# Performance work log

Measured on AMD Instinct MI355X. Metric: run time of the kernel, lower is better.

## Reference

```python
import jax, jax.numpy as jnp
import numpy as np

EPS = 1e-5  # torch GroupNorm default


def setup_inputs() -> dict:
    key = jax.random.key(0)
    ks = jax.random.split(key, 7)
    B, H, W, C = 8, 64, 64, 64
    x = jax.random.normal(ks[0], (B, H, W, C), dtype=jnp.float32)
    temb = jax.random.normal(ks[1], (B, 256), dtype=jnp.float32)
    scale = 0.02
    Wq = jax.random.normal(ks[2], (C, C), dtype=jnp.float32) * scale
    Wk = jax.random.normal(ks[3], (C, C), dtype=jnp.float32) * scale
    Wv = jax.random.normal(ks[4], (C, C), dtype=jnp.float32) * scale
    Wo = jax.random.normal(ks[5], (C, C), dtype=jnp.float32) * scale
    z = jnp.zeros((C,), dtype=jnp.float32)
    return {"x": x, "temb": temb, "Wq": Wq, "bq": z, "Wk": Wk, "bk": z,
            "Wv": Wv, "bv": z, "Wo": Wo, "bo": z}


def reference(x, temb, Wq, bq, Wk, bk, Wv, bv, Wo, bo):
    # x: [B, H, W, C] channels-last. temb is accepted but unused (as in source).
    B, H, W, C = x.shape
    S = H * W
    # normalize(): freshly-built GroupNorm(num_groups=1) with identity affine
    # -> standardize over all non-batch dims.
    mu = jnp.mean(x, axis=(1, 2, 3), keepdims=True)
    var = jnp.var(x, axis=(1, 2, 3), keepdims=True)
    h = (x - mu) * jax.lax.rsqrt(var + EPS)
    hf = h.reshape(B, S, C)
    q = hf @ Wq.T + bq  # [B, S, C]
    k = hf @ Wk.T + bk
    v = hf @ Wv.T + bv
    # full (S x S) score matrix, scaled by C^-0.5, naive softmax
    w = jnp.einsum('bsc,btc->bst', q, k) * (C ** -0.5)
    w = jax.nn.softmax(w, axis=-1)
    o = jnp.einsum('bst,btc->bsc', w, v)  # [B, S, C]
    o = o @ Wo.T + bo
    return x + o.reshape(B, H, W, C)
```

## Files before the change

kernel.cpp:

```cpp
#include <hip/hip_runtime.h>
#include <hip/hip_bf16.h>
#include <math.h>

#define B_ 8
#define S_ 4096
#define C_ 64
#define EPSV 1e-5f

using floatx4  = __attribute__((ext_vector_type(4)))  float;
using floatx16 = __attribute__((ext_vector_type(16))) float;
using bf16x8   = __attribute__((ext_vector_type(8)))  short;

typedef __attribute__((address_space(3))) unsigned int       as3_u32;
typedef __attribute__((address_space(1))) const unsigned int as1_u32;

__device__ __forceinline__ short f2bf(float f) {
    unsigned u = __builtin_bit_cast(unsigned, f);
    u = u + 0x7fffu + ((u >> 16) & 1u);
    return (short)(u >> 16);
}

__device__ __forceinline__ float bf2f(short s) {
    return __builtin_bit_cast(float, ((unsigned)(unsigned short)s) << 16);
}

__device__ __forceinline__ unsigned cvt_pk_bf16(float lo, float hi) {
    unsigned r;
    asm volatile("v_cvt_pk_bf16_f32 %0, %1, %2" : "=v"(r) : "v"(lo), "v"(hi));
    return r;
}

__device__ __forceinline__ void perm32swap(unsigned &a, unsigned &b) {
#if __has_builtin(__builtin_amdgcn_permlane32_swap)
    auto r = __builtin_amdgcn_permlane32_swap((int)a, (int)b, false, false);
    a = (unsigned)r[0];
    b = (unsigned)r[1];
#else
    asm volatile("v_permlane32_swap_b32 %0, %1" : "+v"(a), "+v"(b));
#endif
}

__device__ __forceinline__ bf16x8 ld_w_frag(const float* __restrict__ W, int n, int kk, int g, int c) {
    const float* p = W + (16 * n + c) * C_ + 32 * kk + 8 * g;
    bf16x8 r;
#pragma unroll
    for (int j = 0; j < 8; ++j) r[j] = f2bf(p[j]);
    return r;
}

__global__ __launch_bounds__(256) void stats1_kernel(const float* __restrict__ x,
                                                     float* __restrict__ partial) {
    int b = blockIdx.x >> 5, chunk = blockIdx.x & 31;
    const float4* xb = (const float4*)x + (size_t)b * 65536 + chunk * 2048;
    float s = 0.f, ss = 0.f;
#pragma unroll
    for (int i = 0; i < 8; ++i) {
        float4 v = xb[threadIdx.x + i * 256];
        s  += v.x + v.y + v.z + v.w;
        ss += v.x * v.x + v.y * v.y + v.z * v.z + v.w * v.w;
    }
    for (int off = 32; off > 0; off >>= 1) {
        s  += __shfl_down(s, off);
        ss += __shfl_down(ss, off);
    }
    __shared__ float sm[4], ssm[4];
    int wid = threadIdx.x >> 6, lane = threadIdx.x & 63;
    if (lane == 0) { sm[wid] = s; ssm[wid] = ss; }
    __syncthreads();
    if (threadIdx.x == 0) {
        partial[blockIdx.x * 2]     = sm[0] + sm[1] + sm[2] + sm[3];
        partial[blockIdx.x * 2 + 1] = ssm[0] + ssm[1] + ssm[2] + ssm[3];
    }
}

__global__ __launch_bounds__(512) void stats2_kernel(const float* __restrict__ partial,
                                                     float* __restrict__ stats) {
    int w = threadIdx.x >> 6, lane = threadIdx.x & 63;
    float s = 0.f, ss = 0.f;
    if (lane < 32) {
        s  = partial[(w * 32 + lane) * 2];
        ss = partial[(w * 32 + lane) * 2 + 1];
    }
    for (int off = 16; off > 0; off >>= 1) {
        s  += __shfl_down(s, off);
        ss += __shfl_down(ss, off);
    }
    if (lane == 0) {
        const float invN = 1.0f / (float)(S_ * C_);
        float mu  = s * invN;
        float var = ss * invN - mu * mu;
        stats[w * 2]     = mu;
        stats[w * 2 + 1] = rsqrtf(var + EPSV);
    }
}

__global__ __launch_bounds__(256) void proj_kernel(
    const float* __restrict__ x,
    const float* __restrict__ Wq, const float* __restrict__ bq,
    const float* __restrict__ Wk, const float* __restrict__ bk,
    const float* __restrict__ Wv, const float* __restrict__ bv,
    const float* __restrict__ stats,
    short* __restrict__ qo, char* __restrict__ kws, char* __restrict__ vws) {
    __shared__ char hbuf[8192];
    __shared__ char qimg[8192];
    __shared__ char kimg[8192];
    __shared__ char vimg[8192];

    int b  = blockIdx.x >> 6;
    int t_ = blockIdx.x & 63;
    int s0 = t_ * 64;
    float mu = stats[b * 2], rs = stats[b * 2 + 1];
    const float* xt = x + ((size_t)b * S_ + s0) * C_;
    int t = threadIdx.x;

#pragma unroll
    for (int i = 0; i < 4; ++i) {
        int fi  = t + 256 * i;
        int row = fi >> 4;
        int c4  = fi & 15;
        float4 v = *(const float4*)(xt + row * C_ + c4 * 4);
        unsigned lo = (unsigned)(unsigned short)f2bf((v.x - mu) * rs) |
                      ((unsigned)(unsigned short)f2bf((v.y - mu) * rs) << 16);
        unsigned hi = (unsigned)(unsigned short)f2bf((v.z - mu) * rs) |
                      ((unsigned)(unsigned short)f2bf((v.w - mu) * rs) << 16);
        int off = row * 128 + c4 * 8;
        off ^= (row & 7) << 4;
        *(uint2*)(hbuf + off) = make_uint2(lo, hi);
    }
    __syncthreads();

    int lane = t & 63, w = t >> 6;
    int g = lane >> 4, c = lane & 15;

    auto ld_h = [&](int row, int kcol) -> bf16x8 {
        int off = row * 128 + kcol * 2;
        off ^= (row & 7) << 4;
        return *(const bf16x8*)(hbuf + off);
    };

    bf16x8 ha[2];
    ha[0] = ld_h(16 * w + c, 8 * g);
    ha[1] = ld_h(16 * w + c, 32 + 8 * g);

    const float QSC = 0.125f * 1.44269504088896340736f;

#pragma unroll
    for (int n = 0; n < 4; ++n) {
        floatx4 aq = {0.f, 0.f, 0.f, 0.f}, ak = {0.f, 0.f, 0.f, 0.f};
#pragma unroll
        for (int kk = 0; kk < 2; ++kk) {
            bf16x8 wq = ld_w_frag(Wq, n, kk, g, c);
            bf16x8 wk = ld_w_frag(Wk, n, kk, g, c);
            aq = __builtin_amdgcn_mfma_f32_16x16x32_bf16(ha[kk], wq, aq, 0, 0, 0);
            ak = __builtin_amdgcn_mfma_f32_16x16x32_bf16(ha[kk], wk, ak, 0, 0, 0);
        }
        float bqv = bq[16 * n + c], bkv = bk[16 * n + c];
#pragma unroll
        for (int r = 0; r < 4; ++r) {
            int rr = 16 * w + 4 * g + r;
            *(short*)(qimg + rr * 128 + (16 * n + c) * 2) = f2bf((aq[r] + bqv) * QSC);
            int r32 = rr & 31;
            int koff = (r32 * 128 + (16 * n + c) * 2) ^ ((r32 & 7) << 4);
            *(short*)(kimg + (rr >> 5) * 4096 + koff) = f2bf(ak[r] + bkv);
        }
    }

    bf16x8 wv[2];
    wv[0] = ld_w_frag(Wv, w, 0, g, c);
    wv[1] = ld_w_frag(Wv, w, 1, g, c);
    float bvr[4];
#pragma unroll
    for (int r = 0; r < 4; ++r) bvr[r] = bv[16 * w + 4 * g + r];

#pragma unroll
    for (int n = 0; n < 4; ++n) {
        floatx4 av = {0.f, 0.f, 0.f, 0.f};
#pragma unroll
        for (int kk = 0; kk < 2; ++kk) {
            bf16x8 hb = ld_h(16 * n + c, 32 * kk + 8 * g);
            av = __builtin_amdgcn_mfma_f32_16x16x32_bf16(wv[kk], hb, av, 0, 0, 0);
        }
        int u   = 16 * n + c;
        int u32 = u & 31;
#pragma unroll
        for (int r = 0; r < 4; ++r) {
            int rr = 16 * w + 4 * g + r;
            int voff = (rr * 64 + u32 * 2) ^ (((rr >> 1) & 3) << 4);
            *(short*)(vimg + (u >> 5) * 4096 + voff) = f2bf(av[r] + bvr[r]);
        }
    }
    __syncthreads();

    size_t gb = ((size_t)b * 128 + 2 * t_) * 4096;
    uint4* qdst = (uint4*)(qo + ((size_t)b * S_ + s0) * C_);
#pragma unroll
    for (int i = 0; i < 2; ++i) {
        qdst[t + 256 * i] = *(const uint4*)(qimg + i * 4096 + t * 16);
        *(uint4*)(kws + gb + i * 4096 + t * 16) = *(const uint4*)(kimg + i * 4096 + t * 16);
        *(uint4*)(vws + gb + i * 4096 + t * 16) = *(const uint4*)(vimg + i * 4096 + t * 16);
    }
}

__global__ __launch_bounds__(256, 4) void flash_kernel(
    const short* __restrict__ qm, const char* __restrict__ kws, const char* __restrict__ vws,
    short* __restrict__ Opart, float2* __restrict__ mlpart) {
    __shared__ char lds[16384];

    int bid = blockIdx.x;
    int logical = (bid & 7) * 128 + (bid >> 3);
    int b = logical >> 7;
    int rest = logical & 127;
    int q0 = (rest >> 2) * 128;
    int quarter = rest & 3;
    int t = threadIdx.x;
    int lane = t & 63, w = t >> 6;
    int r5 = lane & 31, hi = lane >> 5;
    int qw = q0 + 32 * w;

    const char* kbase = kws + (size_t)b * 128 * 4096;
    const char* vbase = vws + (size_t)b * 128 * 4096;
    const short* qp = qm + (size_t)b * S_ * C_;

    bf16x8 bq[4];
#pragma unroll
    for (int kk = 0; kk < 4; ++kk)
        bq[kk] = *(const bf16x8*)(qp + (qw + r5) * C_ + 16 * kk + 8 * hi);

    floatx16 oacc[2];
#pragma unroll
    for (int mm = 0; mm < 2; ++mm)
#pragma unroll
        for (int i = 0; i < 16; ++i) oacc[mm][i] = 0.f;
    float m = -64.f, nm = 64.f, l = 0.f;

    const int kxm = (r5 & 7) << 4;
    const int vxm = ((r5 >> 1) & 3) << 4;

    auto STAGE = [&](int bi, int tt) {
        const char* gk = kbase + (size_t)tt * 4096 + t * 16;
        const char* gv = vbase + (size_t)tt * 4096 + t * 16;
        char* lk = lds +        bi * 4096 + t * 16;
        char* lv = lds + 8192 + bi * 4096 + t * 16;
        __builtin_amdgcn_global_load_lds((as1_u32*)gk, (as3_u32*)lk, 16, 0, 0);
        __builtin_amdgcn_global_load_lds((as1_u32*)gv, (as3_u32*)lv, 16, 0, 0);
    };

    auto ld_k = [&](const char* buf, int kk) -> bf16x8 {
        return *(const bf16x8*)(buf + r5 * 128 + ((32 * kk + 16 * hi) ^ kxm));
    };
    auto ld_v = [&](const char* buf, int mm, int s) -> bf16x8 {
        return *(const bf16x8*)(buf + (32 * mm + r5) * 64 + ((32 * s + 16 * hi) ^ vxm));
    };

    auto COMPUTE = [&](int bi) {
        const char* kbuf = lds +        bi * 4096;
        const char* vbuf = lds + 8192 + bi * 4096;
        floatx16 st;
#pragma unroll
        for (int i = 0; i < 16; ++i) st[i] = nm;
        __builtin_amdgcn_s_setprio(1);
#pragma unroll
        for (int kk = 0; kk < 4; ++kk) {
            bf16x8 ak = ld_k(kbuf, kk);
            st = __builtin_amdgcn_mfma_f32_32x32x16_bf16(ak, bq[kk], st, 0, 0, 0);
        }
        __builtin_amdgcn_s_setprio(0);
        bf16x8 av[2][2];
#pragma unroll
        for (int mm = 0; mm < 2; ++mm)
#pragma unroll
            for (int s = 0; s < 2; ++s)
                av[mm][s] = ld_v(vbuf, mm, s);
        float mt = st[0];
#pragma unroll
        for (int i = 1; i < 16; ++i) mt = fmaxf(mt, st[i]);
        mt = fmaxf(mt, __shfl_xor(mt, 32));
        if (!__all(mt <= 8.0f)) {
            float d = fmaxf(mt, 0.f);
            float a = __builtin_amdgcn_exp2f(-d);
            m += d;
            nm = -m;
            l *= a;
#pragma unroll
            for (int mm = 0; mm < 2; ++mm) oacc[mm] *= a;
#pragma unroll
            for (int i = 0; i < 16; ++i) st[i] -= d;
        }
        float e[16], psum = 0.f;
#pragma unroll
        for (int i = 0; i < 16; ++i) e[i] = __builtin_amdgcn_exp2f(st[i]);
#pragma unroll
        for (int i = 0; i < 16; ++i) psum += e[i];
        l += psum;
        unsigned wd[8];
#pragma unroll
        for (int j = 0; j < 8; ++j) wd[j] = cvt_pk_bf16(e[2 * j], e[2 * j + 1]);
        perm32swap(wd[0], wd[2]);
        perm32swap(wd[1], wd[3]);
        perm32swap(wd[4], wd[6]);
        perm32swap(wd[5], wd[7]);
        uint4 u0 = make_uint4(wd[0], wd[1], wd[2], wd[3]);
        uint4 u1 = make_uint4(wd[4], wd[5], wd[6], wd[7]);
        bf16x8 bp0 = __builtin_bit_cast(bf16x8, u0);
        bf16x8 bp1 = __builtin_bit_cast(bf16x8, u1);
        __builtin_amdgcn_s_setprio(1);
#pragma unroll
        for (int mm = 0; mm < 2; ++mm) {
            oacc[mm] = __builtin_amdgcn_mfma_f32_32x32x16_bf16(av[mm][0], bp0, oacc[mm], 0, 0, 0);
            oacc[mm] = __builtin_amdgcn_mfma_f32_32x32x16_bf16(av[mm][1], bp1, oacc[mm], 0, 0, 0);
        }
        __builtin_amdgcn_s_setprio(0);
    };

    const int base = quarter * 32;
    STAGE(0, base);
    __syncthreads();
    for (int r = 0; r < 32; r += 2) {
        STAGE(1, base + r + 1);
        COMPUTE(0);
        __syncthreads();
        if (r + 2 < 32) STAGE(0, base + r + 2);
        COMPUTE(1);
        __syncthreads();
    }

    l += __shfl_xor(l, 32);

    size_t prow = (size_t)(quarter * 8 + b) * S_ + q0;
    if (lane < 32)
        mlpart[prow + 32 * w + r5] = make_float2(m, l);

    short* op = Opart + (prow + 32 * w + r5) * C_;
#pragma unroll
    for (int mm = 0; mm < 2; ++mm) {
#pragma unroll
        for (int j = 0; j < 4; ++j) {
            int ch = 32 * mm + 8 * j + 4 * hi;
            uint2 u = make_uint2(cvt_pk_bf16(oacc[mm][4 * j],     oacc[mm][4 * j + 1]),
                                 cvt_pk_bf16(oacc[mm][4 * j + 2], oacc[mm][4 * j + 3]));
            *(uint2*)(op + ch) = u;
        }
    }
}

__global__ __launch_bounds__(256) void combine_kernel(
    const short* __restrict__ Opart, const float2* __restrict__ mlpart,
    const float* __restrict__ Wo, const float* __restrict__ bo,
    const float* __restrict__ x, float* __restrict__ out) {
    __shared__ char obuf[8192];

    int bid = blockIdx.x;
    int logical = (bid & 7) * 64 + (bid >> 3);
    int b = logical >> 6;
    int q0 = (logical & 63) * 64;
    int t = threadIdx.x;
    int lane = t & 63, w = t >> 6;
    int g = lane >> 4, c = lane & 15;

    const short*  P[4];
    const float2* ml[4];
#pragma unroll
    for (int h = 0; h < 4; ++h) {
        P[h]  = Opart  + ((size_t)(h * 8 + b) * S_ + q0) * C_;
        ml[h] = mlpart + (size_t)(h * 8 + b) * S_ + q0;
    }

#pragma unroll
    for (int i = 0; i < 16; ++i) {
        int idx = t + 256 * i;
        int q = idx >> 6, ch = idx & 63;
        float2 a0 = ml[0][q], a1 = ml[1][q], a2 = ml[2][q], a3 = ml[3][q];
        float M = fmaxf(fmaxf(a0.x, a1.x), fmaxf(a2.x, a3.x));
        float s0 = __builtin_amdgcn_exp2f(a0.x - M);
        float s1 = __builtin_amdgcn_exp2f(a1.x - M);
        float s2 = __builtin_amdgcn_exp2f(a2.x - M);
        float s3 = __builtin_amdgcn_exp2f(a3.x - M);
        float L  = a0.y * s0 + a1.y * s1 + a2.y * s2 + a3.y * s3;
        float o  = (bf2f(P[0][q * 64 + ch]) * s0 + bf2f(P[1][q * 64 + ch]) * s1 +
                    bf2f(P[2][q * 64 + ch]) * s2 + bf2f(P[3][q * 64 + ch]) * s3) / L;
        int off = (q * 128 + ch * 2) ^ ((q & 7) << 4);
        *(short*)(obuf + off) = f2bf(o);
    }
    __syncthreads();

    bf16x8 ao[2];
    {
        int row = 16 * w + c;
        int off0 = (row * 128 + (8 * g) * 2)      ^ ((row & 7) << 4);
        int off1 = (row * 128 + (32 + 8 * g) * 2) ^ ((row & 7) << 4);
        ao[0] = *(const bf16x8*)(obuf + off0);
        ao[1] = *(const bf16x8*)(obuf + off1);
    }
#pragma unroll
    for (int n = 0; n < 4; ++n) {
        floatx4 a = {0.f, 0.f, 0.f, 0.f};
#pragma unroll
        for (int kk = 0; kk < 2; ++kk) {
            bf16x8 bw = ld_w_frag(Wo, n, kk, g, c);
            a = __builtin_amdgcn_mfma_f32_16x16x32_bf16(ao[kk], bw, a, 0, 0, 0);
        }
        float bov = bo[16 * n + c];
#pragma unroll
        for (int r = 0; r < 4; ++r) {
            int srow = q0 + 16 * w + 4 * g + r;
            size_t idx = ((size_t)b * S_ + srow) * C_ + 16 * n + c;
            out[idx] = x[idx] + bov + a[r];
        }
    }
}

extern "C" void kernel_launch(void* const* d_in, const int* in_sizes, int n_in,
                              void* d_out, int out_size, void* d_ws, size_t ws_size,
                              hipStream_t stream) {
    const float* x  = (const float*)d_in[0];
    const float* Wq = (const float*)d_in[2];
    const float* bq = (const float*)d_in[3];
    const float* Wk = (const float*)d_in[4];
    const float* bk = (const float*)d_in[5];
    const float* Wv = (const float*)d_in[6];
    const float* bv = (const float*)d_in[7];
    const float* Wo = (const float*)d_in[8];
    const float* bo = (const float*)d_in[9];
    float* out = (float*)d_out;

    char* ws = (char*)d_ws;
    float*  partial = (float*)ws;
    float*  stats   = (float*)(ws + 2048);
    short*  q   = (short*)(ws + 4096);
    char*   kt  = (char*)(q + (size_t)B_ * S_ * C_);
    char*   vt  = kt + (size_t)B_ * 128 * 4096;
    short*  op  = (short*)(vt + (size_t)B_ * 128 * 4096);
    float2* mlp = (float2*)((char*)op + (size_t)4 * B_ * S_ * C_ * 2);

    stats1_kernel<<<256, 256, 0, stream>>>(x, partial);
    stats2_kernel<<<1, 512, 0, stream>>>(partial, stats);
    proj_kernel<<<B_ * (S_ / 64), 256, 0, stream>>>(x, Wq, bq, Wk, bk, Wv, bv, stats, q, kt, vt);
    flash_kernel<<<B_ * (S_ / 128) * 4, 256, 0, stream>>>(q, kt, vt, op, mlp);
    combine_kernel<<<B_ * (S_ / 64), 256, 0, stream>>>(op, mlp, Wo, bo, x, out);
}
```

Baseline: 80.40 us.

## Fuse split-KV combine and output projection into flash kernel via last-block counter

Removes the separate combine kernel. Each flash block now bumps an atomic counter per (batch, 128-query tile), and the last of the four KV-quarter blocks merges the partial outputs, applies Wo and bo, and adds the residual, working in two 64-row halves that reuse the flash LDS buffer. The counters are zeroed in stats1_kernel. This saves one kernel launch and lets the combine work overlap with other flash blocks, at the cost of threadfences, an atomic per block, and uneven tail work on the last-arriving blocks.

```diff
diff --git a/kernel.cpp b/kernel.cpp
--- a/kernel.cpp
+++ b/kernel.cpp
@@ -49,7 +49,9 @@
 }
 
 __global__ __launch_bounds__(256) void stats1_kernel(const float* __restrict__ x,
-                                                     float* __restrict__ partial) {
+                                                     float* __restrict__ partial,
+                                                     int* __restrict__ cnt) {
+    if (threadIdx.x == 0) cnt[blockIdx.x] = 0;
     int b = blockIdx.x >> 5, chunk = blockIdx.x & 31;
     const float4* xb = (const float4*)x + (size_t)b * 65536 + chunk * 2048;
     float s = 0.f, ss = 0.f;
@@ -203,8 +205,11 @@
 
 __global__ __launch_bounds__(256, 4) void flash_kernel(
     const short* __restrict__ qm, const char* __restrict__ kws, const char* __restrict__ vws,
-    short* __restrict__ Opart, float2* __restrict__ mlpart) {
+    short* __restrict__ Opart, float2* __restrict__ mlpart, int* __restrict__ cnt,
+    const float* __restrict__ Wo, const float* __restrict__ bo,
+    const float* __restrict__ x, float* __restrict__ out) {
     __shared__ char lds[16384];
+    __shared__ int lastflag;
 
     int bid = blockIdx.x;
     int logical = (bid & 7) * 128 + (bid >> 3);
@@ -341,21 +346,17 @@
             *(uint2*)(op + ch) = u;
         }
     }
-}
-
-__global__ __launch_bounds__(256) void combine_kernel(
-    const short* __restrict__ Opart, const float2* __restrict__ mlpart,
-    const float* __restrict__ Wo, const float* __restrict__ bo,
-    const float* __restrict__ x, float* __restrict__ out) {
-    __shared__ char obuf[8192];
-
-    int bid = blockIdx.x;
-    int logical = (bid & 7) * 64 + (bid >> 3);
-    int b = logical >> 6;
-    int q0 = (logical & 63) * 64;
-    int t = threadIdx.x;
-    int lane = t & 63, w = t >> 6;
-    int g = lane >> 4, c = lane & 15;
+
+    __threadfence();
+    __syncthreads();
+    if (t == 0) {
+        int old = __hip_atomic_fetch_add(&cnt[(b << 5) + (rest >> 2)], 1,
+                                         __ATOMIC_ACQ_REL, __HIP_MEMORY_SCOPE_AGENT);
+        lastflag = (old == 3);
+    }
+    __syncthreads();
+    if (!lastflag) return;
+    __threadfence();
 
     const short*  P[4];
     const float2* ml[4];
@@ -364,48 +365,56 @@
         P[h]  = Opart  + ((size_t)(h * 8 + b) * S_ + q0) * C_;
         ml[h] = mlpart + (size_t)(h * 8 + b) * S_ + q0;
     }
-
-#pragma unroll
-    for (int i = 0; i < 16; ++i) {
-        int idx = t + 256 * i;
-        int q = idx >> 6, ch = idx & 63;
-        float2 a0 = ml[0][q], a1 = ml[1][q], a2 = ml[2][q], a3 = ml[3][q];
-        float M = fmaxf(fmaxf(a0.x, a1.x), fmaxf(a2.x, a3.x));
-        float s0 = __builtin_amdgcn_exp2f(a0.x - M);
-        float s1 = __builtin_amdgcn_exp2f(a1.x - M);
-        float s2 = __builtin_amdgcn_exp2f(a2.x - M);
-        float s3 = __builtin_amdgcn_exp2f(a3.x - M);
-        float L  = a0.y * s0 + a1.y * s1 + a2.y * s2 + a3.y * s3;
-        float o  = (bf2f(P[0][q * 64 + ch]) * s0 + bf2f(P[1][q * 64 + ch]) * s1 +
-                    bf2f(P[2][q * 64 + ch]) * s2 + bf2f(P[3][q * 64 + ch]) * s3) / L;
-        int off = (q * 128 + ch * 2) ^ ((q & 7) << 4);
-        *(short*)(obuf + off) = f2bf(o);
-    }
-    __syncthreads();
-
-    bf16x8 ao[2];
-    {
-        int row = 16 * w + c;
-        int off0 = (row * 128 + (8 * g) * 2)      ^ ((row & 7) << 4);
-        int off1 = (row * 128 + (32 + 8 * g) * 2) ^ ((row & 7) << 4);
-        ao[0] = *(const bf16x8*)(obuf + off0);
-        ao[1] = *(const bf16x8*)(obuf + off1);
-    }
-#pragma unroll
-    for (int n = 0; n < 4; ++n) {
-        floatx4 a = {0.f, 0.f, 0.f, 0.f};
-#pragma unroll
-        for (int kk = 0; kk < 2; ++kk) {
-            bf16x8 bw = ld_w_frag(Wo, n, kk, g, c);
-            a = __builtin_amdgcn_mfma_f32_16x16x32_bf16(ao[kk], bw, a, 0, 0, 0);
-        }
-        float bov = bo[16 * n + c];
-#pragma unroll
-        for (int r = 0; r < 4; ++r) {
-            int srow = q0 + 16 * w + 4 * g + r;
-            size_t idx = ((size_t)b * S_ + srow) * C_ + 16 * n + c;
-            out[idx] = x[idx] + bov + a[r];
-        }
+    int g = lane >> 4, c = lane & 15;
+    char* obuf = lds;
+
+#pragma unroll
+    for (int half = 0; half < 2; ++half) {
+        int qh = 64 * half;
+#pragma unroll
+        for (int i = 0; i < 16; ++i) {
+            int idx = t + 256 * i;
+            int qq = idx >> 6, ch = idx & 63;
+            int q = qh + qq;
+            float2 a0 = ml[0][q], a1 = ml[1][q], a2 = ml[2][q], a3 = ml[3][q];
+            float M = fmaxf(fmaxf(a0.x, a1.x), fmaxf(a2.x, a3.x));
+            float s0 = __builtin_amdgcn_exp2f(a0.x - M);
+            float s1 = __builtin_amdgcn_exp2f(a1.x - M);
+            float s2 = __builtin_amdgcn_exp2f(a2.x - M);
+            float s3 = __builtin_amdgcn_exp2f(a3.x - M);
+            float L  = a0.y * s0 + a1.y * s1 + a2.y * s2 + a3.y * s3;
+            float o  = (bf2f(P[0][q * 64 + ch]) * s0 + bf2f(P[1][q * 64 + ch]) * s1 +
+                        bf2f(P[2][q * 64 + ch]) * s2 + bf2f(P[3][q * 64 + ch]) * s3) / L;
+            int off = (qq * 128 + ch * 2) ^ ((qq & 7) << 4);
+            *(short*)(obuf + off) = f2bf(o);
+        }
+        __syncthreads();
+
+        bf16x8 ao[2];
+        {
+            int row = 16 * w + c;
+            int off0 = (row * 128 + (8 * g) * 2)      ^ ((row & 7) << 4);
+            int off1 = (row * 128 + (32 + 8 * g) * 2) ^ ((row & 7) << 4);
+            ao[0] = *(const bf16x8*)(obuf + off0);
+            ao[1] = *(const bf16x8*)(obuf + off1);
+        }
+#pragma unroll
+        for (int n = 0; n < 4; ++n) {
+            floatx4 a = {0.f, 0.f, 0.f, 0.f};
+#pragma unroll
+            for (int kk = 0; kk < 2; ++kk) {
+                bf16x8 bw = ld_w_frag(Wo, n, kk, g, c);
+                a = __builtin_amdgcn_mfma_f32_16x16x32_bf16(ao[kk], bw, a, 0, 0, 0);
+            }
+            float bov = bo[16 * n + c];
+#pragma unroll
+            for (int r = 0; r < 4; ++r) {
+                int srow = q0 + qh + 16 * w + 4 * g + r;
+                size_t idx = ((size_t)b * S_ + srow) * C_ + 16 * n + c;
+                out[idx] = x[idx] + bov + a[r];
+            }
+        }
+        __syncthreads();
     }
 }
 
@@ -431,10 +440,10 @@
     char*   vt  = kt + (size_t)B_ * 128 * 4096;
     short*  op  = (short*)(vt + (size_t)B_ * 128 * 4096);
     float2* mlp = (float2*)((char*)op + (size_t)4 * B_ * S_ * C_ * 2);
-
-    stats1_kernel<<<256, 256, 0, stream>>>(x, partial);
+    int*    cnt = (int*)((char*)mlp + (size_t)4 * B_ * S_ * 8);
+
+    stats1_kernel<<<256, 256, 0, stream>>>(x, partial, cnt);
     stats2_kernel<<<1, 512, 0, stream>>>(partial, stats);
     proj_kernel<<<B_ * (S_ / 64), 256, 0, stream>>>(x, Wq, bq, Wk, bk, Wv, bv, stats, q, kt, vt);
-    flash_kernel<<<B_ * (S_ / 128) * 4, 256, 0, stream>>>(q, kt, vt, op, mlp);
-    combine_kernel<<<B_ * (S_ / 64), 256, 0, stream>>>(op, mlp, Wo, bo, x, out);
-}
+    flash_kernel<<<B_ * (S_ / 128) * 4, 256, 0, stream>>>(q, kt, vt, op, mlp, cnt, Wo, bo, x, out);
+}
```

Result: slower. 306.4 us (+281.1%).
